# Kernel optimization log

Hardware: AMD Instinct MI355X
Metric: run time of the kernel (lower is better)

## Reference

```python
import jax, jax.numpy as jnp
import numpy as np

NQ = 4
DIM = 2 ** NQ  # 16 basis states for the 4-qubit patch circuit


def _cnot_chain_perm():
    # Combined basis permutation for CNOT(0,1); CNOT(1,2); CNOT(2,3),
    # with wire i = bit (NQ-1-i) of the basis index (wire 0 most significant).
    idx = np.arange(DIM)
    perm = idx
    for c in range(NQ - 1):
        t = c + 1
        cbit = (idx >> (NQ - 1 - c)) & 1
        single = idx ^ (cbit << (NQ - 1 - t))  # involution: flip target iff control=1
        perm = perm[single]
    return perm

_BITS = np.array([[(b >> (NQ - 1 - i)) & 1 for i in range(NQ)] for b in range(DIM)])
CNOT_PERM = jnp.asarray(_cnot_chain_perm())
ZSIGN = jnp.asarray(1.0 - 2.0 * _BITS, dtype=jnp.float32)  # (DIM, NQ): PauliZ eigenvalues per basis/qubit


def _quantum(patches, params):
    """Exact statevector sim of: RY(x_i) -> CNOT chain -> RZ(p0) -> CNOT chain -> RZ(p1) -> <Z_i>.
    patches: (N, 4) angles; params: (2, 4). Returns (N, 4) expectation values."""
    half = 0.5 * patches
    amp = jnp.stack([jnp.cos(half), jnp.sin(half)], axis=-1)  # (N, 4, 2) per-qubit RY|0> amplitudes
    state = jnp.einsum('na,nb,nc,nd->nabcd', amp[:, 0], amp[:, 1], amp[:, 2], amp[:, 3])
    state = state.reshape(-1, DIM).astype(jnp.complex64)
    for row in range(2):
        state = state[:, CNOT_PERM]                    # CNOT chain = basis permutation
        phase = jnp.exp(-0.5j * (ZSIGN @ params[row]))  # RZ diagonal, shared across batch
        state = state * phase
    probs = jnp.real(state) ** 2 + jnp.imag(state) ** 2
    return probs @ ZSIGN  # (N, 4)


def setup_inputs() -> dict:
    key = jax.random.key(0)
    ks = jax.random.split(key, 5)
    B = 8192
    return {
        'x': jax.random.uniform(ks[0], (B, 1, 28, 28), jnp.float32),
        'params': jax.random.normal(ks[1], (2, NQ), jnp.float32),
        'W1': jax.random.normal(ks[2], (256, 784), jnp.float32) * 0.03,
        'b1': jnp.zeros((256,), jnp.float32),
        'W2': jax.random.normal(ks[3], (128, 256), jnp.float32) * 0.06,
        'b2': jnp.zeros((128,), jnp.float32),
        'W3': jax.random.normal(ks[4], (10, 128), jnp.float32) * 0.08,
        'b3': jnp.zeros((10,), jnp.float32),
    }


def reference(x, params, W1, b1, W2, b2, W3, b3):
    B = x.shape[0]
    # Extract 2x2 patches (row-major within patch, row-major patch order) -> (B*196, 4)
    patches = x[:, 0].reshape(B, 14, 2, 14, 2).transpose(0, 1, 3, 2, 4).reshape(B * 196, 4)
    feats = _quantum(patches, params).reshape(B, 196 * 4)  # cat of per-patch 4-vectors
    h = jax.nn.relu(feats @ W1.T + b1)   # Dropout is identity in eval mode
    h = jax.nn.relu(h @ W2.T + b2)
    logits = h @ W3.T + b3
    return jax.nn.log_softmax(logits, axis=-1)
```

## Files before the change

kernel.cpp:

```cpp
#include <hip/hip_runtime.h>
#include <stdint.h>

typedef __attribute__((ext_vector_type(8))) short short8;
typedef __attribute__((ext_vector_type(4))) float f32x4;

#define DEVI __device__ __forceinline__

DEVI ushort f2bf(float f) {
  union { float f; uint32_t u; } v; v.f = f;
  uint32_t r = v.u + 0x7fffu + ((v.u >> 16) & 1u);
  return (ushort)(r >> 16);
}

DEVI ushort4 pack4(float a, float b, float c, float d) {
  ushort4 o; o.x = f2bf(a); o.y = f2bf(b); o.z = f2bf(c); o.w = f2bf(d);
  return o;
}

#define LDB 72
#define H1LD 280

__global__ __launch_bounds__(512, 2) void mega_kernel(
    const float* __restrict__ x, const float* __restrict__ W1,
    const float* __restrict__ b1, const float* __restrict__ W2,
    const float* __restrict__ b2, const float* __restrict__ W3,
    const float* __restrict__ b3, float* __restrict__ out) {
  __shared__ __align__(16) ushort As[32 * LDB];
  __shared__ __align__(16) ushort Bs[256 * LDB];
  __shared__ __align__(16) ushort h1t[32 * H1LD];
  __shared__ __align__(16) float W3s[1280];

  const int tid = threadIdx.x;
  const int lane = tid & 63;
  const int w = tid >> 6;
  const int m0g = blockIdx.x * 32;

  const int arow = tid >> 4, pl = tid & 15;

  float2 xt, xb;
  bool aval;
  float4 bw[8];

  auto loadA1 = [&](int kt) {
    const int q = kt * 16 + pl;
    aval = (q < 196);
    if (aval) {
      const int i = q / 14, j = q - i * 14;
      const float* p = x + (size_t)(m0g + arow) * 784 + i * 56 + j * 2;
      xt = *(const float2*)p;
      xb = *(const float2*)(p + 28);
    }
  };
  auto loadB1 = [&](int kt) {
    const int k0 = kt * 64;
#pragma unroll
    for (int c = 0; c < 8; ++c) {
      const int flat = c * 512 + tid, r = flat >> 4, sl = flat & 15;
      if (k0 + sl * 4 < 784)
        bw[c] = *(const float4*)(W1 + (size_t)r * 784 + k0 + sl * 4);
      else
        bw[c] = make_float4(0.f, 0.f, 0.f, 0.f);
    }
  };
  auto writeT1 = [&]() {
    if (aval) {
      float c0 = __cosf(xt.x), c1 = __cosf(xt.y);
      float c2 = __cosf(xb.x), c3 = __cosf(xb.y);
      *(ushort4*)(As + arow * LDB + pl * 4) = pack4(c0, c1, c0 * c2, c1 * c3);
    } else {
      ushort4 z; z.x = 0; z.y = 0; z.z = 0; z.w = 0;
      *(ushort4*)(As + arow * LDB + pl * 4) = z;
    }
#pragma unroll
    for (int c = 0; c < 8; ++c) {
      const int flat = c * 512 + tid, r = flat >> 4, sl = flat & 15;
      *(ushort4*)(Bs + r * LDB + sl * 4) = pack4(bw[c].x, bw[c].y, bw[c].z, bw[c].w);
    }
  };

  f32x4 acc[2][2];
#pragma unroll
  for (int m = 0; m < 2; ++m)
#pragma unroll
    for (int n = 0; n < 2; ++n) {
      f32x4 z = {0.f, 0.f, 0.f, 0.f};
      acc[m][n] = z;
    }

  loadA1(0);
  loadB1(0);
  for (int kt = 0; kt < 13; ++kt) {
    writeT1();
    __syncthreads();
    if (kt < 12) { loadA1(kt + 1); loadB1(kt + 1); }
#pragma unroll
    for (int ks = 0; ks < 2; ++ks) {
      short8 af[2], bf[2];
#pragma unroll
      for (int m = 0; m < 2; ++m)
        af[m] = *(const short8*)(As + (m * 16 + (lane & 15)) * LDB + ks * 32 + (lane >> 4) * 8);
#pragma unroll
      for (int n = 0; n < 2; ++n)
        bf[n] = *(const short8*)(Bs + (w * 32 + n * 16 + (lane & 15)) * LDB + ks * 32 + (lane >> 4) * 8);
#pragma unroll
      for (int m = 0; m < 2; ++m)
#pragma unroll
        for (int n = 0; n < 2; ++n)
          acc[m][n] = __builtin_amdgcn_mfma_f32_16x16x32_bf16(af[m], bf[n], acc[m][n], 0, 0, 0);
    }
    __syncthreads();
  }

#pragma unroll
  for (int n = 0; n < 2; ++n) {
    const int col = w * 32 + n * 16 + (lane & 15);
    const float bval = b1[col];
#pragma unroll
    for (int m = 0; m < 2; ++m)
#pragma unroll
      for (int r = 0; r < 4; ++r) {
        const int row = m * 16 + (lane >> 4) * 4 + r;
        h1t[row * H1LD + col] = f2bf(fmaxf(acc[m][n][r] + bval, 0.f));
      }
  }
  for (int i = tid; i < 1280; i += 512) W3s[i] = W3[i];
  __syncthreads();

  float4 bw2[4];
  auto loadB2 = [&](int kt) {
    const int k0 = kt * 64;
#pragma unroll
    for (int c = 0; c < 4; ++c) {
      const int flat = c * 512 + tid, r = flat >> 4, sl = flat & 15;
      bw2[c] = *(const float4*)(W2 + (size_t)r * 256 + k0 + sl * 4);
    }
  };
  auto writeT2 = [&]() {
#pragma unroll
    for (int c = 0; c < 4; ++c) {
      const int flat = c * 512 + tid, r = flat >> 4, sl = flat & 15;
      *(ushort4*)(Bs + r * LDB + sl * 4) = pack4(bw2[c].x, bw2[c].y, bw2[c].z, bw2[c].w);
    }
  };

  f32x4 acc2[2];
#pragma unroll
  for (int m = 0; m < 2; ++m) {
    f32x4 z = {0.f, 0.f, 0.f, 0.f};
    acc2[m] = z;
  }

  loadB2(0);
  for (int kt = 0; kt < 4; ++kt) {
    writeT2();
    __syncthreads();
    if (kt < 3) loadB2(kt + 1);
#pragma unroll
    for (int ks = 0; ks < 2; ++ks) {
      short8 bf = *(const short8*)(Bs + (w * 16 + (lane & 15)) * LDB + ks * 32 + (lane >> 4) * 8);
#pragma unroll
      for (int m = 0; m < 2; ++m) {
        short8 af = *(const short8*)(h1t + (m * 16 + (lane & 15)) * H1LD + kt * 64 + ks * 32 + (lane >> 4) * 8);
        acc2[m] = __builtin_amdgcn_mfma_f32_16x16x32_bf16(af, bf, acc2[m], 0, 0, 0);
      }
    }
    __syncthreads();
  }

  float* h2f = (float*)h1t;
  {
    const int col = w * 16 + (lane & 15);
    const float bval = b2[col];
#pragma unroll
    for (int m = 0; m < 2; ++m)
#pragma unroll
      for (int r = 0; r < 4; ++r) {
        const int row = m * 16 + (lane >> 4) * 4 + r;
        h2f[row * 132 + col] = fmaxf(acc2[m][r] + bval, 0.f);
      }
  }
  __syncthreads();

  {
    const int r = tid >> 4, p = tid & 15;
    float a10[10];
#pragma unroll
    for (int n = 0; n < 10; ++n) a10[n] = 0.f;
#pragma unroll
    for (int e = 0; e < 8; ++e) {
      const int k = e * 16 + p;
      const float hv = h2f[r * 132 + k];
#pragma unroll
      for (int n = 0; n < 10; ++n) a10[n] = fmaf(hv, W3s[n * 128 + k], a10[n]);
    }
#pragma unroll
    for (int n = 0; n < 10; ++n) {
      a10[n] += __shfl_xor(a10[n], 1);
      a10[n] += __shfl_xor(a10[n], 2);
      a10[n] += __shfl_xor(a10[n], 4);
      a10[n] += __shfl_xor(a10[n], 8);
    }
    if (p == 0) {
#pragma unroll
      for (int n = 0; n < 10; ++n) a10[n] += b3[n];
      float mx = a10[0];
#pragma unroll
      for (int n = 1; n < 10; ++n) mx = fmaxf(mx, a10[n]);
      float s = 0.f;
#pragma unroll
      for (int n = 0; n < 10; ++n) s += __expf(a10[n] - mx);
      const float lse = mx + __logf(s);
      float* po = out + (size_t)(m0g + r) * 10;
#pragma unroll
      for (int n = 0; n < 10; ++n) po[n] = a10[n] - lse;
    }
  }
}

extern "C" void kernel_launch(void* const* d_in, const int* in_sizes, int n_in,
                              void* d_out, int out_size, void* d_ws, size_t ws_size,
                              hipStream_t stream) {
  const float* x  = (const float*)d_in[0];
  const float* W1 = (const float*)d_in[2];
  const float* b1 = (const float*)d_in[3];
  const float* W2 = (const float*)d_in[4];
  const float* b2 = (const float*)d_in[5];
  const float* W3 = (const float*)d_in[6];
  const float* b3 = (const float*)d_in[7];
  float* out = (float*)d_out;

  hipLaunchKernelGGL(mega_kernel, dim3(256), dim3(512), 0, stream,
                     x, W1, b1, W2, b2, W3, b3, out);
}
```

Before: 33.04 us.

## Pre-convert weights to bf16 in a prep kernel and double-buffer LDS tiles

Adds a prep kernel that converts W1 (padded to 832 columns) and W2 to bf16 in workspace once per call, so the main kernel loads half the bytes and skips per-block conversion. The main kernel now double-buffers A and B tiles in shared memory, so each k-step needs one barrier instead of two and loads overlap the MFMA work. The cost is an extra kernel launch, roughly double the LDS use (which may cut occupancy from two blocks per CU), and extra workspace traffic.

```diff
diff --git a/kernel.cpp b/kernel.cpp
--- a/kernel.cpp
+++ b/kernel.cpp
@@ -17,16 +17,35 @@
   return o;
 }
 
+__global__ __launch_bounds__(256) void prep_w_kernel(
+    const float* __restrict__ W1, const float* __restrict__ W2,
+    ushort* __restrict__ w1b, ushort* __restrict__ w2b) {
+  int t = blockIdx.x * 256 + threadIdx.x;
+  if (t < 256 * 832) {
+    int r = t / 832, c = t - r * 832;
+    w1b[t] = (c < 784) ? f2bf(W1[r * 784 + c]) : (ushort)0;
+  } else {
+    int u = t - 256 * 832;
+    w2b[u] = f2bf(W2[u]);
+  }
+}
+
 #define LDB 72
 #define H1LD 280
 
-__global__ __launch_bounds__(512, 2) void mega_kernel(
-    const float* __restrict__ x, const float* __restrict__ W1,
-    const float* __restrict__ b1, const float* __restrict__ W2,
+struct Stage1 {
+  float2 xt, xb;
+  int aval;
+  uint4 bv[4];
+};
+
+__global__ __launch_bounds__(512) void mega2_kernel(
+    const float* __restrict__ x, const ushort* __restrict__ w1b,
+    const float* __restrict__ b1, const ushort* __restrict__ w2b,
     const float* __restrict__ b2, const float* __restrict__ W3,
     const float* __restrict__ b3, float* __restrict__ out) {
-  __shared__ __align__(16) ushort As[32 * LDB];
-  __shared__ __align__(16) ushort Bs[256 * LDB];
+  __shared__ __align__(16) ushort As[2][32 * LDB];
+  __shared__ __align__(16) ushort Bs[2][256 * LDB];
   __shared__ __align__(16) ushort h1t[32 * H1LD];
   __shared__ __align__(16) float W3s[1280];
 
@@ -37,44 +56,35 @@
 
   const int arow = tid >> 4, pl = tid & 15;
 
-  float2 xt, xb;
-  bool aval;
-  float4 bw[8];
-
-  auto loadA1 = [&](int kt) {
+  auto loadT1 = [&](Stage1& S, int kt) {
     const int q = kt * 16 + pl;
-    aval = (q < 196);
-    if (aval) {
+    S.aval = (q < 196);
+    if (S.aval) {
       const int i = q / 14, j = q - i * 14;
       const float* p = x + (size_t)(m0g + arow) * 784 + i * 56 + j * 2;
-      xt = *(const float2*)p;
-      xb = *(const float2*)(p + 28);
-    }
-  };
-  auto loadB1 = [&](int kt) {
+      S.xt = *(const float2*)p;
+      S.xb = *(const float2*)(p + 28);
+    }
     const int k0 = kt * 64;
 #pragma unroll
-    for (int c = 0; c < 8; ++c) {
-      const int flat = c * 512 + tid, r = flat >> 4, sl = flat & 15;
-      if (k0 + sl * 4 < 784)
-        bw[c] = *(const float4*)(W1 + (size_t)r * 784 + k0 + sl * 4);
-      else
-        bw[c] = make_float4(0.f, 0.f, 0.f, 0.f);
-    }
-  };
-  auto writeT1 = [&]() {
-    if (aval) {
-      float c0 = __cosf(xt.x), c1 = __cosf(xt.y);
-      float c2 = __cosf(xb.x), c3 = __cosf(xb.y);
-      *(ushort4*)(As + arow * LDB + pl * 4) = pack4(c0, c1, c0 * c2, c1 * c3);
+    for (int c = 0; c < 4; ++c) {
+      const int flat = c * 512 + tid, r = flat >> 3, s = flat & 7;
+      S.bv[c] = *(const uint4*)(w1b + (size_t)r * 832 + k0 + s * 8);
+    }
+  };
+  auto writeT1 = [&](int buf, const Stage1& S) {
+    if (S.aval) {
+      float c0 = __cosf(S.xt.x), c1 = __cosf(S.xt.y);
+      float c2 = __cosf(S.xb.x), c3 = __cosf(S.xb.y);
+      *(ushort4*)(&As[buf][arow * LDB + pl * 4]) = pack4(c0, c1, c0 * c2, c1 * c3);
     } else {
       ushort4 z; z.x = 0; z.y = 0; z.z = 0; z.w = 0;
-      *(ushort4*)(As + arow * LDB + pl * 4) = z;
-    }
-#pragma unroll
-    for (int c = 0; c < 8; ++c) {
-      const int flat = c * 512 + tid, r = flat >> 4, sl = flat & 15;
-      *(ushort4*)(Bs + r * LDB + sl * 4) = pack4(bw[c].x, bw[c].y, bw[c].z, bw[c].w);
+      *(ushort4*)(&As[buf][arow * LDB + pl * 4]) = z;
+    }
+#pragma unroll
+    for (int c = 0; c < 4; ++c) {
+      const int flat = c * 512 + tid, r = flat >> 3, s = flat & 7;
+      *(uint4*)(&Bs[buf][r * LDB + s * 8]) = S.bv[c];
     }
   };
 
@@ -87,28 +97,41 @@
       acc[m][n] = z;
     }
 
-  loadA1(0);
-  loadB1(0);
-  for (int kt = 0; kt < 13; ++kt) {
-    writeT1();
-    __syncthreads();
-    if (kt < 12) { loadA1(kt + 1); loadB1(kt + 1); }
+  auto mma1 = [&](int buf) {
 #pragma unroll
     for (int ks = 0; ks < 2; ++ks) {
       short8 af[2], bf[2];
 #pragma unroll
       for (int m = 0; m < 2; ++m)
-        af[m] = *(const short8*)(As + (m * 16 + (lane & 15)) * LDB + ks * 32 + (lane >> 4) * 8);
+        af[m] = *(const short8*)(&As[buf][(m * 16 + (lane & 15)) * LDB + ks * 32 + (lane >> 4) * 8]);
 #pragma unroll
       for (int n = 0; n < 2; ++n)
-        bf[n] = *(const short8*)(Bs + (w * 32 + n * 16 + (lane & 15)) * LDB + ks * 32 + (lane >> 4) * 8);
+        bf[n] = *(const short8*)(&Bs[buf][(w * 32 + n * 16 + (lane & 15)) * LDB + ks * 32 + (lane >> 4) * 8]);
 #pragma unroll
       for (int m = 0; m < 2; ++m)
 #pragma unroll
         for (int n = 0; n < 2; ++n)
           acc[m][n] = __builtin_amdgcn_mfma_f32_16x16x32_bf16(af[m], bf[n], acc[m][n], 0, 0, 0);
     }
+  };
+
+  Stage1 S0, S1;
+  loadT1(S0, 0);
+  loadT1(S1, 1);
+  writeT1(0, S0);
+  __syncthreads();
+
+  for (int kt = 0; kt < 13; kt += 2) {
+    mma1(0);
+    if (kt + 2 < 13) loadT1(S0, kt + 2);
+    if (kt + 1 < 13) writeT1(1, S1);
     __syncthreads();
+    if (kt + 1 < 13) {
+      mma1(1);
+      if (kt + 3 < 13) loadT1(S1, kt + 3);
+      if (kt + 2 < 13) writeT1(0, S0);
+      __syncthreads();
+    }
   }
 
 #pragma unroll
@@ -124,22 +147,20 @@
       }
   }
   for (int i = tid; i < 1280; i += 512) W3s[i] = W3[i];
-  __syncthreads();
-
-  float4 bw2[4];
+
+  uint4 t2[2];
   auto loadB2 = [&](int kt) {
-    const int k0 = kt * 64;
-#pragma unroll
-    for (int c = 0; c < 4; ++c) {
-      const int flat = c * 512 + tid, r = flat >> 4, sl = flat & 15;
-      bw2[c] = *(const float4*)(W2 + (size_t)r * 256 + k0 + sl * 4);
-    }
-  };
-  auto writeT2 = [&]() {
-#pragma unroll
-    for (int c = 0; c < 4; ++c) {
-      const int flat = c * 512 + tid, r = flat >> 4, sl = flat & 15;
-      *(ushort4*)(Bs + r * LDB + sl * 4) = pack4(bw2[c].x, bw2[c].y, bw2[c].z, bw2[c].w);
+#pragma unroll
+    for (int c = 0; c < 2; ++c) {
+      const int flat = c * 512 + tid, r = flat >> 3, s = flat & 7;
+      t2[c] = *(const uint4*)(w2b + (size_t)r * 256 + kt * 64 + s * 8);
+    }
+  };
+  auto writeB2 = [&](int buf) {
+#pragma unroll
+    for (int c = 0; c < 2; ++c) {
+      const int flat = c * 512 + tid, r = flat >> 3, s = flat & 7;
+      *(uint4*)(&Bs[buf][r * LDB + s * 8]) = t2[c];
     }
   };
 
@@ -150,20 +171,27 @@
     acc2[m] = z;
   }
 
-  loadB2(0);
-  for (int kt = 0; kt < 4; ++kt) {
-    writeT2();
-    __syncthreads();
-    if (kt < 3) loadB2(kt + 1);
+  auto mma2 = [&](int buf, int kt) {
 #pragma unroll
     for (int ks = 0; ks < 2; ++ks) {
-      short8 bf = *(const short8*)(Bs + (w * 16 + (lane & 15)) * LDB + ks * 32 + (lane >> 4) * 8);
+      short8 bf = *(const short8*)(&Bs[buf][(w * 16 + (lane & 15)) * LDB + ks * 32 + (lane >> 4) * 8]);
 #pragma unroll
       for (int m = 0; m < 2; ++m) {
-        short8 af = *(const short8*)(h1t + (m * 16 + (lane & 15)) * H1LD + kt * 64 + ks * 32 + (lane >> 4) * 8);
+        short8 af = *(const short8*)(&h1t[(m * 16 + (lane & 15)) * H1LD + kt * 64 + ks * 32 + (lane >> 4) * 8]);
         acc2[m] = __builtin_amdgcn_mfma_f32_16x16x32_bf16(af, bf, acc2[m], 0, 0, 0);
       }
     }
+  };
+
+  loadB2(0);
+  writeB2(0);
+  __syncthreads();
+
+#pragma unroll
+  for (int kt = 0; kt < 4; ++kt) {
+    if (kt < 3) loadB2(kt + 1);
+    mma2(kt & 1, kt);
+    if (kt < 3) writeB2((kt + 1) & 1);
     __syncthreads();
   }
 
@@ -229,6 +257,11 @@
   const float* b3 = (const float*)d_in[7];
   float* out = (float*)d_out;
 
-  hipLaunchKernelGGL(mega_kernel, dim3(256), dim3(512), 0, stream,
-                     x, W1, b1, W2, b2, W3, b3, out);
-}
+  char* ws = (char*)d_ws;
+  ushort* w1b = (ushort*)(ws);
+  ushort* w2b = (ushort*)(ws + 425984);
+
+  hipLaunchKernelGGL(prep_w_kernel, dim3(960), dim3(256), 0, stream, W1, W2, w1b, w2b);
+  hipLaunchKernelGGL(mega2_kernel, dim3(256), dim3(512), 0, stream,
+                     x, w1b, b1, w2b, b2, W3, b3, out);
+}
```

New measurement: 51.59 us. 1.56x slower.

## Double-buffer LDS tiles, halve rows per block, use hardware bf16 pack

Applied to the files above, without the earlier changes.

Rows per block drop from 32 to 16 and the grid doubles to 512 blocks, so more blocks can spread across CUs. The layer-1 and layer-2 GEMM loops now double-buffer the shared-memory tiles: the next tile is loaded from global and written to the other buffer while MFMAs run on the current one, which cuts each iteration to a single barrier. The h1, W3 and h2 scratch areas are placed in unused parts of the B buffers to save LDS, and float-to-bf16 packing uses the v_cvt_pk_bf16_f32 instruction. The cost is that W1 and W2 are fetched from L2 twice as often across the grid. A launch bound of 4 blocks limits registers per thread, which risks spilling the 8 prefetched float4 values.

```diff
diff --git a/kernel.cpp b/kernel.cpp
--- a/kernel.cpp
+++ b/kernel.cpp
@@ -12,46 +12,51 @@
   return (ushort)(r >> 16);
 }
 
-DEVI ushort4 pack4(float a, float b, float c, float d) {
-  ushort4 o; o.x = f2bf(a); o.y = f2bf(b); o.z = f2bf(c); o.w = f2bf(d);
+DEVI uint32_t cvtpk(float lo, float hi) {
+  uint32_t r;
+  asm("v_cvt_pk_bf16_f32 %0, %1, %2" : "=v"(r) : "v"(lo), "v"(hi));
+  return r;
+}
+DEVI uint2 pack4(float a, float b, float c, float d) {
+  uint2 o; o.x = cvtpk(a, b); o.y = cvtpk(c, d);
   return o;
 }
 
-#define LDB 72
-#define H1LD 280
-
-__global__ __launch_bounds__(512, 2) void mega_kernel(
+#define LDA 72
+#define H1LD 264
+
+__global__ __launch_bounds__(512, 4) void mega3_kernel(
     const float* __restrict__ x, const float* __restrict__ W1,
     const float* __restrict__ b1, const float* __restrict__ W2,
     const float* __restrict__ b2, const float* __restrict__ W3,
     const float* __restrict__ b3, float* __restrict__ out) {
-  __shared__ __align__(16) ushort As[32 * LDB];
-  __shared__ __align__(16) ushort Bs[256 * LDB];
-  __shared__ __align__(16) ushort h1t[32 * H1LD];
-  __shared__ __align__(16) float W3s[1280];
+  __shared__ __align__(16) ushort As[2][16 * LDA];
+  __shared__ __align__(16) ushort Bs[2][256 * LDA];
+
+  ushort* h1t = &Bs[0][128 * LDA];
+  float* W3s = (float*)&Bs[1][128 * LDA];
+  float* h2f = (float*)&Bs[1][128 * LDA + 2560];
 
   const int tid = threadIdx.x;
   const int lane = tid & 63;
   const int w = tid >> 6;
-  const int m0g = blockIdx.x * 32;
+  const int m0 = blockIdx.x * 16;
 
   const int arow = tid >> 4, pl = tid & 15;
 
-  float2 xt, xb;
-  bool aval;
+  float2 atop, abot;
   float4 bw[8];
 
-  auto loadA1 = [&](int kt) {
-    const int q = kt * 16 + pl;
-    aval = (q < 196);
-    if (aval) {
-      const int i = q / 14, j = q - i * 14;
-      const float* p = x + (size_t)(m0g + arow) * 784 + i * 56 + j * 2;
-      xt = *(const float2*)p;
-      xb = *(const float2*)(p + 28);
-    }
-  };
-  auto loadB1 = [&](int kt) {
+  auto loadT1 = [&](int kt) {
+    if (tid < 256) {
+      const int q = kt * 16 + pl;
+      if (q < 196) {
+        const int i = q / 14, j = q - i * 14;
+        const float* p = x + (size_t)(m0 + arow) * 784 + i * 56 + j * 2;
+        atop = *(const float2*)p;
+        abot = *(const float2*)(p + 28);
+      }
+    }
     const int k0 = kt * 64;
 #pragma unroll
     for (int c = 0; c < 8; ++c) {
@@ -62,53 +67,56 @@
         bw[c] = make_float4(0.f, 0.f, 0.f, 0.f);
     }
   };
-  auto writeT1 = [&]() {
-    if (aval) {
-      float c0 = __cosf(xt.x), c1 = __cosf(xt.y);
-      float c2 = __cosf(xb.x), c3 = __cosf(xb.y);
-      *(ushort4*)(As + arow * LDB + pl * 4) = pack4(c0, c1, c0 * c2, c1 * c3);
-    } else {
-      ushort4 z; z.x = 0; z.y = 0; z.z = 0; z.w = 0;
-      *(ushort4*)(As + arow * LDB + pl * 4) = z;
+  auto writeT1 = [&](int buf, int kt) {
+    if (tid < 256) {
+      const int q = kt * 16 + pl;
+      if (q < 196) {
+        float c0 = __cosf(atop.x), c1 = __cosf(atop.y);
+        float c2 = __cosf(abot.x), c3 = __cosf(abot.y);
+        *(uint2*)(&As[buf][arow * LDA + pl * 4]) = pack4(c0, c1, c0 * c2, c1 * c3);
+      } else {
+        uint2 z; z.x = 0; z.y = 0;
+        *(uint2*)(&As[buf][arow * LDA + pl * 4]) = z;
+      }
     }
 #pragma unroll
     for (int c = 0; c < 8; ++c) {
       const int flat = c * 512 + tid, r = flat >> 4, sl = flat & 15;
-      *(ushort4*)(Bs + r * LDB + sl * 4) = pack4(bw[c].x, bw[c].y, bw[c].z, bw[c].w);
-    }
-  };
-
-  f32x4 acc[2][2];
-#pragma unroll
-  for (int m = 0; m < 2; ++m)
-#pragma unroll
-    for (int n = 0; n < 2; ++n) {
-      f32x4 z = {0.f, 0.f, 0.f, 0.f};
-      acc[m][n] = z;
-    }
-
-  loadA1(0);
-  loadB1(0);
+      *(uint2*)(&Bs[buf][r * LDA + sl * 4]) =
+          pack4(bw[c].x, bw[c].y, bw[c].z, bw[c].w);
+    }
+  };
+
+  f32x4 acc[2];
+#pragma unroll
+  for (int n = 0; n < 2; ++n) {
+    f32x4 z = {0.f, 0.f, 0.f, 0.f};
+    acc[n] = z;
+  }
+
+  auto mma1 = [&](int buf) {
+#pragma unroll
+    for (int ks = 0; ks < 2; ++ks) {
+      short8 af = *(const short8*)(&As[buf][(lane & 15) * LDA + ks * 32 + (lane >> 4) * 8]);
+#pragma unroll
+      for (int n = 0; n < 2; ++n) {
+        const int cdx = w * 32 + n * 16 + (lane & 15);
+        short8 bf = *(const short8*)(&Bs[buf][cdx * LDA + ks * 32 + (lane >> 4) * 8]);
+        acc[n] = __builtin_amdgcn_mfma_f32_16x16x32_bf16(af, bf, acc[n], 0, 0, 0);
+      }
+    }
+  };
+
+  loadT1(0);
+  writeT1(0, 0);
+  __syncthreads();
+  int cur = 0;
   for (int kt = 0; kt < 13; ++kt) {
-    writeT1();
+    if (kt + 1 < 13) loadT1(kt + 1);
+    mma1(cur);
+    if (kt + 1 < 13) writeT1(cur ^ 1, kt + 1);
     __syncthreads();
-    if (kt < 12) { loadA1(kt + 1); loadB1(kt + 1); }
-#pragma unroll
-    for (int ks = 0; ks < 2; ++ks) {
-      short8 af[2], bf[2];
-#pragma unroll
-      for (int m = 0; m < 2; ++m)
-        af[m] = *(const short8*)(As + (m * 16 + (lane & 15)) * LDB + ks * 32 + (lane >> 4) * 8);
-#pragma unroll
-      for (int n = 0; n < 2; ++n)
-        bf[n] = *(const short8*)(Bs + (w * 32 + n * 16 + (lane & 15)) * LDB + ks * 32 + (lane >> 4) * 8);
-#pragma unroll
-      for (int m = 0; m < 2; ++m)
-#pragma unroll
-        for (int n = 0; n < 2; ++n)
-          acc[m][n] = __builtin_amdgcn_mfma_f32_16x16x32_bf16(af[m], bf[n], acc[m][n], 0, 0, 0);
-    }
-    __syncthreads();
+    cur ^= 1;
   }
 
 #pragma unroll
@@ -116,15 +124,12 @@
     const int col = w * 32 + n * 16 + (lane & 15);
     const float bval = b1[col];
 #pragma unroll
-    for (int m = 0; m < 2; ++m)
-#pragma unroll
-      for (int r = 0; r < 4; ++r) {
-        const int row = m * 16 + (lane >> 4) * 4 + r;
-        h1t[row * H1LD + col] = f2bf(fmaxf(acc[m][n][r] + bval, 0.f));
-      }
+    for (int r = 0; r < 4; ++r) {
+      const int row = (lane >> 4) * 4 + r;
+      h1t[row * H1LD + col] = f2bf(fmaxf(acc[n][r] + bval, 0.f));
+    }
   }
   for (int i = tid; i < 1280; i += 512) W3s[i] = W3[i];
-  __syncthreads();
 
   float4 bw2[4];
   auto loadB2 = [&](int kt) {
@@ -135,60 +140,58 @@
       bw2[c] = *(const float4*)(W2 + (size_t)r * 256 + k0 + sl * 4);
     }
   };
-  auto writeT2 = [&]() {
+  auto writeB2 = [&](int buf) {
 #pragma unroll
     for (int c = 0; c < 4; ++c) {
       const int flat = c * 512 + tid, r = flat >> 4, sl = flat & 15;
-      *(ushort4*)(Bs + r * LDB + sl * 4) = pack4(bw2[c].x, bw2[c].y, bw2[c].z, bw2[c].w);
-    }
-  };
-
-  f32x4 acc2[2];
-#pragma unroll
-  for (int m = 0; m < 2; ++m) {
+      *(uint2*)(&Bs[buf][r * LDA + sl * 4]) =
+          pack4(bw2[c].x, bw2[c].y, bw2[c].z, bw2[c].w);
+    }
+  };
+
+  f32x4 acc2;
+  {
     f32x4 z = {0.f, 0.f, 0.f, 0.f};
-    acc2[m] = z;
-  }
+    acc2 = z;
+  }
+  auto mma2 = [&](int buf, int kt) {
+#pragma unroll
+    for (int ks = 0; ks < 2; ++ks) {
+      short8 af = *(const short8*)(&h1t[(lane & 15) * H1LD + kt * 64 + ks * 32 + (lane >> 4) * 8]);
+      const int cdx = w * 16 + (lane & 15);
+      short8 bf = *(const short8*)(&Bs[buf][cdx * LDA + ks * 32 + (lane >> 4) * 8]);
+      acc2 = __builtin_amdgcn_mfma_f32_16x16x32_bf16(af, bf, acc2, 0, 0, 0);
+    }
+  };
 
   loadB2(0);
+  writeB2(0);
+  __syncthreads();
+#pragma unroll
   for (int kt = 0; kt < 4; ++kt) {
-    writeT2();
+    if (kt < 3) loadB2(kt + 1);
+    mma2(kt & 1, kt);
+    if (kt < 3) writeB2((kt + 1) & 1);
     __syncthreads();
-    if (kt < 3) loadB2(kt + 1);
-#pragma unroll
-    for (int ks = 0; ks < 2; ++ks) {
-      short8 bf = *(const short8*)(Bs + (w * 16 + (lane & 15)) * LDB + ks * 32 + (lane >> 4) * 8);
-#pragma unroll
-      for (int m = 0; m < 2; ++m) {
-        short8 af = *(const short8*)(h1t + (m * 16 + (lane & 15)) * H1LD + kt * 64 + ks * 32 + (lane >> 4) * 8);
-        acc2[m] = __builtin_amdgcn_mfma_f32_16x16x32_bf16(af, bf, acc2[m], 0, 0, 0);
-      }
-    }
-    __syncthreads();
-  }
-
-  float* h2f = (float*)h1t;
+  }
+
   {
     const int col = w * 16 + (lane & 15);
     const float bval = b2[col];
 #pragma unroll
-    for (int m = 0; m < 2; ++m)
-#pragma unroll
-      for (int r = 0; r < 4; ++r) {
-        const int row = m * 16 + (lane >> 4) * 4 + r;
-        h2f[row * 132 + col] = fmaxf(acc2[m][r] + bval, 0.f);
-      }
+    for (int r = 0; r < 4; ++r)
+      h2f[((lane >> 4) * 4 + r) * 132 + col] = fmaxf(acc2[r] + bval, 0.f);
   }
   __syncthreads();
 
   {
-    const int r = tid >> 4, p = tid & 15;
+    const int r = tid >> 5, p = tid & 31;
     float a10[10];
 #pragma unroll
     for (int n = 0; n < 10; ++n) a10[n] = 0.f;
 #pragma unroll
-    for (int e = 0; e < 8; ++e) {
-      const int k = e * 16 + p;
+    for (int e = 0; e < 4; ++e) {
+      const int k = e * 32 + p;
       const float hv = h2f[r * 132 + k];
 #pragma unroll
       for (int n = 0; n < 10; ++n) a10[n] = fmaf(hv, W3s[n * 128 + k], a10[n]);
@@ -199,6 +202,7 @@
       a10[n] += __shfl_xor(a10[n], 2);
       a10[n] += __shfl_xor(a10[n], 4);
       a10[n] += __shfl_xor(a10[n], 8);
+      a10[n] += __shfl_xor(a10[n], 16);
     }
     if (p == 0) {
 #pragma unroll
@@ -210,7 +214,7 @@
 #pragma unroll
       for (int n = 0; n < 10; ++n) s += __expf(a10[n] - mx);
       const float lse = mx + __logf(s);
-      float* po = out + (size_t)(m0g + r) * 10;
+      float* po = out + (size_t)(m0 + r) * 10;
 #pragma unroll
       for (int n = 0; n < 10; ++n) po[n] = a10[n] - lse;
     }
@@ -229,6 +233,6 @@
   const float* b3 = (const float*)d_in[7];
   float* out = (float*)d_out;
 
-  hipLaunchKernelGGL(mega_kernel, dim3(256), dim3(512), 0, stream,
+  hipLaunchKernelGGL(mega3_kernel, dim3(512), dim3(512), 0, stream,
                      x, W1, b1, W2, b2, W3, b3, out);
 }
```

After: 36.26 us. 1.1x slower.
